# Performance work log

Measured on AMD Instinct MI355X. Metric: run time of the kernel, lower is better.

Reference implementation:

```python
import jax, jax.numpy as jnp
import numpy as np

N, E = 50000, 400000
IN, HID, HEADS, OUT, EDIM = 128, 16, 8, 128, 32


def _lin(key, fan_in, fan_out, bias=True):
    k1, k2 = jax.random.split(key)
    s = 1.0 / np.sqrt(fan_in)
    W = jax.random.uniform(k1, (fan_in, fan_out), jnp.float32, -s, s)
    if bias:
        b = jax.random.uniform(k2, (fan_out,), jnp.float32, -s, s)
        return W, b
    return W


def setup_inputs() -> dict:
    key = jax.random.key(0)
    ks = jax.random.split(key, 16)
    x = jax.random.normal(ks[0], (N, IN), jnp.float32)
    edge_index = jax.random.randint(ks[1], (2, E), 0, N, jnp.int64)
    edge_feats = jax.random.normal(ks[2], (E, EDIM), jnp.float32)
    H1 = HEADS * HID  # 128
    Wq1, bq1 = _lin(ks[3], IN, H1)
    Wk1, bk1 = _lin(ks[4], IN, H1)
    Wv1, bv1 = _lin(ks[5], IN, H1)
    We1 = _lin(ks[6], EDIM, H1, bias=False)
    Ws1, bs1 = _lin(ks[7], IN, H1)
    Wq2, bq2 = _lin(ks[8], H1, OUT)
    Wk2, bk2 = _lin(ks[9], H1, OUT)
    Wv2, bv2 = _lin(ks[10], H1, OUT)
    We2 = _lin(ks[11], EDIM, OUT, bias=False)
    Ws2, bs2 = _lin(ks[12], H1, OUT)
    return dict(x=x, edge_index=edge_index, edge_feats=edge_feats,
                Wq1=Wq1, bq1=bq1, Wk1=Wk1, bk1=bk1, Wv1=Wv1, bv1=bv1, We1=We1, Ws1=Ws1, bs1=bs1,
                Wq2=Wq2, bq2=bq2, Wk2=Wk2, bk2=bk2, Wv2=Wv2, bv2=bv2, We2=We2, Ws2=Ws2, bs2=bs2)


def transformer_conv(x, src, dst, e, Wq, bq, Wk, bk, Wv, bv, We, Ws, bs, heads, ch, concat):
    # PyG TransformerConv: project at nodes, gather to edges.
    n = x.shape[0]
    q = (x @ Wq + bq).reshape(n, heads, ch)[dst]          # [E,H,C]
    k = (x @ Wk + bk).reshape(n, heads, ch)[src]
    v = (x @ Wv + bv).reshape(n, heads, ch)[src]
    ee = (e @ We).reshape(-1, heads, ch)                   # edge conditioning
    k = k + ee
    v = v + ee
    alpha = (q * k).sum(-1) / jnp.sqrt(jnp.asarray(ch, x.dtype))  # [E,H]
    # per-destination segment softmax
    m = jax.ops.segment_max(alpha, dst, num_segments=n)
    m = jnp.where(jnp.isfinite(m), m, 0.0)
    ea = jnp.exp(alpha - m[dst])
    denom = jax.ops.segment_sum(ea, dst, num_segments=n)
    attn = ea / jnp.maximum(denom[dst], 1e-16)
    out = jax.ops.segment_sum(attn[:, :, None] * v, dst, num_segments=n)  # [N,H,C]
    out = out.reshape(n, heads * ch) if concat else out.mean(axis=1)
    return out + x @ Ws + bs  # root_weight skip


def reference(x, edge_index, edge_feats,
              Wq1, bq1, Wk1, bk1, Wv1, bv1, We1, Ws1, bs1,
              Wq2, bq2, Wk2, bk2, Wv2, bv2, We2, Ws2, bs2):
    src, dst = edge_index[0], edge_index[1]
    h = jax.nn.relu(transformer_conv(x, src, dst, edge_feats,
                                     Wq1, bq1, Wk1, bk1, Wv1, bv1, We1, Ws1, bs1,
                                     HEADS, HID, True))
    # dropout p=0.0 (eval) -> identity
    out = jax.nn.relu(transformer_conv(h, src, dst, edge_feats,
                                       Wq2, bq2, Wk2, bk2, Wv2, bv2, We2, Ws2, bs2,
                                       1, OUT, False))
    return out
```

## Files before the change

kernel.cpp:

```cpp
#include <hip/hip_runtime.h>


using u16 = unsigned short;
using u32 = unsigned int;

#define NODES 50000
#define EDGES 400000
#define NB196 196

typedef __attribute__((ext_vector_type(8))) short bf16x8;
typedef __attribute__((ext_vector_type(4))) float f32x4;

__device__ __forceinline__ float bflo(u32 u) { return __uint_as_float(u << 16); }
__device__ __forceinline__ float bfhi(u32 u) { return __uint_as_float(u & 0xffff0000u); }
__device__ __forceinline__ u16 f2bf(float f) {
    u32 u = __float_as_uint(f);
    u += 0x7fffu + ((u >> 16) & 1u);
    return (u16)(u >> 16);
}
__device__ __forceinline__ u32 pack2(float a, float b) {
    return (u32)f2bf(a) | ((u32)f2bf(b) << 16);
}
__device__ __forceinline__ float rdv(const void* p, int i, int f) {
    return f ? ((const float*)p)[i]
             : __uint_as_float(((u32) reinterpret_cast<const u16*>(p)[i]) << 16);
}

#if __has_builtin(__builtin_amdgcn_fdot2_f32_bf16)
typedef __attribute__((ext_vector_type(2))) __bf16 bf2;
__device__ __forceinline__ float dot2bf(u32 a, u32 b, float c) {
    return __builtin_amdgcn_fdot2_f32_bf16(__builtin_bit_cast(bf2, a),
                                           __builtin_bit_cast(bf2, b), c, false);
}
#else
__device__ __forceinline__ float dot2bf(u32 a, u32 b, float c) {
    return fmaf(bflo(a), bflo(b), fmaf(bfhi(a), bfhi(b), c));
}
#endif

__device__ __forceinline__ float fexp2(float x) {
#if __has_builtin(__builtin_amdgcn_exp2f)
    return __builtin_amdgcn_exp2f(x);
#else
    return exp2f(x);
#endif
}

template <int CTRL>
__device__ __forceinline__ float dpp_addf(float x) {
    int y = __builtin_amdgcn_update_dpp(0, __float_as_int(x), CTRL, 0xF, 0xF, true);
    return x + __int_as_float(y);
}
template <int GRP>
__device__ __forceinline__ float grp_sum(float p, int lane) {
    p = dpp_addf<0xB1>(p);
    p = dpp_addf<0x4E>(p);
    p = dpp_addf<0x141>(p);
    if (GRP == 64) {
        p = dpp_addf<0x140>(p);
        p += __int_as_float(__builtin_amdgcn_ds_swizzle(__float_as_int(p), 0x401F));
        p += __int_as_float(__builtin_amdgcn_ds_bpermute((lane ^ 32) << 2,
                                                         __float_as_int(p)));
    }
    return p;
}

template <int SRC>
__device__ __forceinline__ u32 bcast8u(u32 x) {
    return (u32)__builtin_amdgcn_ds_swizzle((int)x, 0x18 | (SRC << 5));
}

__global__ __launch_bounds__(256) void fill_sentinel(float* __restrict__ out, int n, float val) {
    int i = blockIdx.x * 256 + threadIdx.x;
    if (i < n) out[i] = val;
}

__global__ __launch_bounds__(64) void detect_fmt(const u32* __restrict__ xw,
                                                 const int* __restrict__ eraw,
                                                 int* __restrict__ flags) {
    int lane = threadIdx.x;
    u32 e = (xw[lane] >> 7) & 0xffu;
    unsigned long long sane = __ballot(e >= 90u && e <= 141u);
    unsigned long long zodd = __ballot(eraw[1 + 2 * lane] == 0);
    if (lane == 0) {
        flags[0] = (sane == ~0ull) ? 0 : 1;
        flags[1] = (zodd == ~0ull) ? 1 : 0;
    }
}

#define CXB 3125
#define CDB 1563
__global__ __launch_bounds__(256) void convert_count(
    const void* __restrict__ X, const int* __restrict__ raw,
    const int* __restrict__ flags, u16* __restrict__ xbf,
    int* __restrict__ deg, int total, int E) {
    int b = blockIdx.x;
    if (b < CXB) {
        int i = (b * 256 + threadIdx.x) * 8;
        if (i >= total) return;
        if (flags[0]) {
            const float* xf = (const float*)X + i;
            float4 lo = *reinterpret_cast<const float4*>(xf);
            float4 hi = *reinterpret_cast<const float4*>(xf + 4);
            uint4 val = make_uint4(pack2(lo.x, lo.y), pack2(lo.z, lo.w),
                                   pack2(hi.x, hi.y), pack2(hi.z, hi.w));
            *reinterpret_cast<uint4*>(xbf + i) = val;
        } else {
            *reinterpret_cast<uint4*>(xbf + i) =
                *reinterpret_cast<const uint4*>((const u16*)X + i);
        }
    } else {
        int e = (b - CXB) * 256 + threadIdx.x;
        if (e < E) {
            int f = flags[1];
            int d = f ? raw[2 * (E + e)] : raw[E + e];
            if ((unsigned)d < (unsigned)NODES) atomicAdd(&deg[d], 1);
        }
    }
}

struct TPtrs {
    const void* src[8];
    u16*        dst[8];
    int         K[8];
};
struct WqeP {
    const void *Wq1, *We1, *bq1, *Wq2, *We2, *bq2;
    u16 *WtA, *WtB, *Wt2;
    float *bqe1, *bqe2;
    uint2 *WeP1, *WeP2;
};

__device__ __forceinline__ void wqe_item(const WqeP& Q, int idx, int f) {
    if (idx < 32768) {
        int col = idx >> 7, i = idx & 127;
        int hh = col >> 5, d = col & 31;
        float s = 0.f;
#pragma unroll
        for (int c = 0; c < 16; ++c)
            s += rdv(Q.Wq1, i * 128 + hh * 16 + c, f) * rdv(Q.We1, d * 128 + hh * 16 + c, f);
        if (col < 128) Q.WtA[col * 128 + i] = f2bf(s);
        else           Q.WtB[(col - 128) * 128 + i] = f2bf(s);
    } else if (idx < 49152) {
        int t = idx - 32768;
        int col = t >> 7, i = t & 127;
        float s = 0.f;
        if (col < 32) {
            for (int c = 0; c < 128; ++c)
                s += rdv(Q.Wq2, i * 128 + c, f) * rdv(Q.We2, col * 128 + c, f);
        }
        Q.Wt2[col * 128 + i] = f2bf(s * 0.125f);
    } else if (idx < 49408) {
        int col = idx - 49152;
        int hh = col >> 5, d = col & 31;
        float s = 0.f;
#pragma unroll
        for (int c = 0; c < 16; ++c)
            s += rdv(Q.bq1, hh * 16 + c, f) * rdv(Q.We1, d * 128 + hh * 16 + c, f);
        Q.bqe1[col] = s;
    } else if (idx < 49536) {
        int d = idx - 49408;
        float s = 0.f;
        if (d < 32)
            for (int c = 0; c < 128; ++c)
                s += rdv(Q.bq2, c, f) * rdv(Q.We2, d * 128 + c, f);
        Q.bqe2[d] = s * 0.125f;
    } else if (idx < 50560) {
        int ent = idx - 49536;
        int t = ent >> 6, l = ent & 63, c0 = 2 * l;
        u32 xv = pack2(rdv(Q.We1, (2 * t) * 128 + c0, f),
                       rdv(Q.We1, (2 * t + 1) * 128 + c0, f));
        u32 yv = pack2(rdv(Q.We1, (2 * t) * 128 + c0 + 1, f),
                       rdv(Q.We1, (2 * t + 1) * 128 + c0 + 1, f));
        Q.WeP1[ent] = make_uint2(xv, yv);
    } else if (idx < 51584) {
        int ent = idx - 50560;
        int t = ent >> 6, l = ent & 63, c0 = 2 * l;
        u32 xv = pack2(rdv(Q.We2, (2 * t) * 128 + c0, f),
                       rdv(Q.We2, (2 * t + 1) * 128 + c0, f));
        u32 yv = pack2(rdv(Q.We2, (2 * t) * 128 + c0 + 1, f),
                       rdv(Q.We2, (2 * t + 1) * 128 + c0 + 1, f));
        Q.WeP2[ent] = make_uint2(xv, yv);
    }
}

__global__ __launch_bounds__(256) void prep_w(TPtrs P, WqeP Q, const int* __restrict__ flags) {
    int f = flags[0];
    int b = blockIdx.x;
    if (b < 32) {
        int m = b >> 2;
        int quarter = 16384 >> 2;
        u16* d = P.dst[m];
        int base = (b & 3) * quarter;
        const float* sf = (const float*)P.src[m];
        const u16*   sb = (const u16*)P.src[m];
        for (int idx = base + threadIdx.x; idx < base + quarter; idx += 256) {
            int k = idx >> 7, n = idx & 127;
            d[n * 128 + k] = f ? f2bf(sf[idx]) : sb[idx];
        }
        return;
    }
    int idx = (b - 32) * 256 + threadIdx.x;
    if (idx < 51584) wqe_item(Q, idx, f);
}

__device__ __forceinline__ int block_scan256(int v) {
    __shared__ int ws[4];
    int t = threadIdx.x, lane = t & 63, w = t >> 6;
    int x = v;
#pragma unroll
    for (int off = 1; off < 64; off <<= 1) {
        int y = __shfl_up(x, off, 64);
        if (lane >= off) x += y;
    }
    if (lane == 63) ws[w] = x;
    __syncthreads();
#pragma unroll
    for (int j = 0; j < 3; ++j)
        if (j < w) x += ws[j];
    return x;
}

__global__ __launch_bounds__(256) void scan_a(const int* __restrict__ deg,
                                              int* __restrict__ bsum, int n) {
    int i = blockIdx.x * 256 + threadIdx.x;
    int v = (i < n) ? deg[i] : 0;
    int incl = block_scan256(v);
    if (threadIdx.x == 255) bsum[blockIdx.x] = incl;
}

__global__ __launch_bounds__(256) void scan_b(int* __restrict__ bsum, int nb) {
    int t = threadIdx.x;
    int v = (t < nb) ? bsum[t] : 0;
    int incl = block_scan256(v);
    if (t < nb) bsum[t] = incl - v;
}

__global__ __launch_bounds__(256) void scan_c(const int* __restrict__ deg,
                                              const int* __restrict__ bsum,
                                              int* __restrict__ row_ptr,
                                              int* __restrict__ cursor, int n) {
    int b = blockIdx.x;
    int i = b * 256 + threadIdx.x;
    int v = (i < n) ? deg[i] : 0;
    int incl = block_scan256(v) + bsum[b];
    if (i < n) {
        row_ptr[i + 1] = incl;
        cursor[i] = incl - v;
    }
    if (i == 0) row_ptr[0] = 0;
}

__global__ __launch_bounds__(256) void fill_csr(const int* __restrict__ raw,
                                                const int* __restrict__ flags,
                                                int* __restrict__ cursor,
                                                int* __restrict__ srcs,
                                                int* __restrict__ eids, int E) {
    int e = blockIdx.x * 256 + threadIdx.x;
    if (e < E) {
        int f = flags[1];
        int d = f ? raw[2 * (E + e)] : raw[E + e];
        int s = f ? raw[2 * e] : raw[e];
        if ((unsigned)d < (unsigned)NODES && (unsigned)s < (unsigned)NODES) {
            int pos = atomicAdd(&cursor[d], 1);
            if ((unsigned)pos < (unsigned)E) { srcs[pos] = s; eids[pos] = e; }
        }
    }
}

__global__ __launch_bounds__(256) void gather_ef(const int* __restrict__ eids,
                                                 const void* __restrict__ EF,
                                                 const int* __restrict__ flags,
                                                 u16* __restrict__ EFG, int E) {
    int t = blockIdx.x * 256 + threadIdx.x;
    int pos = t >> 2, seg = t & 3;
    if (pos >= E) return;
    int e = eids[pos];
    uint4 val;
    if (flags[0]) {
        const float* src = (const float*)EF + (size_t)e * 32 + seg * 8;
        float4 lo = *reinterpret_cast<const float4*>(src);
        float4 hi = *reinterpret_cast<const float4*>(src + 4);
        val = make_uint4(pack2(lo.x, lo.y), pack2(lo.z, lo.w),
                         pack2(hi.x, hi.y), pack2(hi.z, hi.w));
    } else {
        val = *reinterpret_cast<const uint4*>((const u16*)EF + (size_t)e * 32 + seg * 8);
    }
    *reinterpret_cast<uint4*>(EFG + (size_t)pos * 32 + seg * 8) = val;
}

struct GemmSets {
    const u16*  Wt[6];
    const void* bias[6];
    u16*        O[6];
    int         bf32[6];
    int         pitch[6];
    float       oscale[6];
};

__global__ __launch_bounds__(256) void gemm128m(
    const u16* __restrict__ A, const int* __restrict__ flags, GemmSets S,
    int nsets, int M) {
    constexpr int K = 128;
    constexpr int PAD = K + 8;
    constexpr int KV = K / 8;
    __shared__ u16 Asl[64 * PAD];
    __shared__ u16 Bsl[128 * PAD];

    int fin = flags[0];
    int m0 = blockIdx.x * 64;

    for (int idx = threadIdx.x; idx < 64 * KV; idx += 256) {
        int r = idx / KV, cv = idx % KV;
        int gr = m0 + r;
        uint4 val = make_uint4(0, 0, 0, 0);
        if (gr < M) val = *reinterpret_cast<const uint4*>(A + (size_t)gr * K + cv * 8);
        *reinterpret_cast<uint4*>(&Asl[r * PAD + cv * 8]) = val;
    }

    int lane = threadIdx.x & 63, wv = threadIdx.x >> 6;
    int l15 = lane & 15;
    int quad = lane >> 4;
    int kq = quad * 8;
    int row = m0 + wv * 16 + l15;

    for (int si = 0; si < nsets; ++si) {
        const u16*  Wt   = S.Wt[si];
        const void* bias = S.bias[si];
        u16*        O    = S.O[si];
        int   pitch = S.pitch[si];
        float os    = S.oscale[si];
        int   f     = S.bf32[si] ? 1 : fin;

        __syncthreads();
        for (int idx = threadIdx.x; idx < 128 * KV; idx += 256) {
            int r = idx / KV, cv = idx % KV;
            *reinterpret_cast<uint4*>(&Bsl[r * PAD + cv * 8]) =
                *reinterpret_cast<const uint4*>(Wt + r * K + cv * 8);
        }
        __syncthreads();

        f32x4 b4[8];
#pragma unroll
        for (int nt = 0; nt < 8; ++nt) {
            int col0 = nt * 16 + quad * 4;
            if (bias) {
                if (f) {
                    b4[nt] = *reinterpret_cast<const f32x4*>((const float*)bias + col0);
                } else {
                    uint2 bu = *reinterpret_cast<const uint2*>((const u16*)bias + col0);
                    b4[nt][0] = bflo(bu.x); b4[nt][1] = bfhi(bu.x);
                    b4[nt][2] = bflo(bu.y); b4[nt][3] = bfhi(bu.y);
                }
            } else {
                b4[nt][0] = b4[nt][1] = b4[nt][2] = b4[nt][3] = 0.f;
            }
        }

        f32x4 acc[8] = {};
#pragma unroll
        for (int k0 = 0; k0 < K; k0 += 32) {
            bf16x8 xf = *reinterpret_cast<const bf16x8*>(&Asl[(wv * 16 + l15) * PAD + k0 + kq]);
#pragma unroll
            for (int nt = 0; nt < 8; ++nt) {
                bf16x8 wf = *reinterpret_cast<const bf16x8*>(&Bsl[(nt * 16 + l15) * PAD + k0 + kq]);
                acc[nt] = __builtin_amdgcn_mfma_f32_16x16x32_bf16(wf, xf, acc[nt], 0, 0, 0);
            }
        }

        if (row < M) {
            u16* Orow = O + (size_t)row * pitch;
#pragma unroll
            for (int nt = 0; nt < 8; ++nt) {
                uint2 pk;
                pk.x = pack2((acc[nt][0] + b4[nt][0]) * os, (acc[nt][1] + b4[nt][1]) * os);
                pk.y = pack2((acc[nt][2] + b4[nt][2]) * os, (acc[nt][3] + b4[nt][3]) * os);
                *reinterpret_cast<uint2*>(Orow + nt * 16 + quad * 4) = pk;
            }
        }
    }
}

template <int HEADS, int F32OUT>
__global__ __launch_bounds__(256) void attn_kernel(
    const int* __restrict__ row_ptr, const int* __restrict__ srcs,
    const u16* __restrict__ Q, const u16* __restrict__ KV,
    const u16* __restrict__ EFG,
    const u16* __restrict__ QWA, const u16* __restrict__ QWB,
    const u16* __restrict__ SK, const uint2* __restrict__ WeP,
    void* __restrict__ OUT, int nn) {
    int wv = threadIdx.x >> 6, lane = threadIdx.x & 63;
    int node = blockIdx.x * 4 + wv;
    if (node >= nn) return;
    int h = lane >> 3, j = lane & 7;
    int c0 = lane * 2;
    constexpr int GRP = (HEADS == 8) ? 8 : 64;

    u32 qb = *reinterpret_cast<const u32*>(Q + (size_t)node * 128 + c0);
    const u16* qp = (HEADS == 8)
        ? ((h < 4 ? QWA : QWB) + (size_t)node * 128 + (h & 3) * 32 + j * 4)
        : (QWA + (size_t)node * 128 + j * 4);
    uint2 qwu = *reinterpret_cast<const uint2*>(qp);

    int beg = __builtin_amdgcn_readfirstlane(row_ptr[node]);
    int end = __builtin_amdgcn_readfirstlane(row_ptr[node + 1]);

    float l_run = 0.f, a0 = 0.f, a1 = 0.f;
    float f0 = 0.f, f1 = 0.f, f2 = 0.f, f3 = 0.f;

    auto edge_step = [&](u32 kbv, u32 vbv, uint2 ebv, bool valid) {
        float p = dot2bf(qb, kbv,
                 dot2bf(qwu.x, ebv.x,
                 dot2bf(qwu.y, ebv.y, 0.f)));
        p = grp_sum<GRP>(p, lane);
        float w = fexp2(p);
        if (!valid) w = 0.f;
        l_run += w;
        a0 = fmaf(w, bflo(vbv), a0);
        a1 = fmaf(w, bfhi(vbv), a1);
        f0 = fmaf(w, bflo(ebv.x), f0); f1 = fmaf(w, bfhi(ebv.x), f1);
        f2 = fmaf(w, bflo(ebv.y), f2); f3 = fmaf(w, bfhi(ebv.y), f3);
    };

    int i = beg;
    for (; i + 8 <= end; i += 8) {
        u32 kb[8], vb[8]; uint2 eb[8];
#pragma unroll
        for (int t = 0; t < 8; ++t) {
            int s = srcs[i + t];
            const u16* kp = KV + (size_t)s * 256;
            kb[t] = *reinterpret_cast<const u32*>(kp + c0);
            vb[t] = *reinterpret_cast<const u32*>(kp + 128 + c0);
            eb[t] = *reinterpret_cast<const uint2*>(EFG + (size_t)(i + t) * 32 + j * 4);
        }
#pragma unroll
        for (int t = 0; t < 8; ++t) edge_step(kb[t], vb[t], eb[t], true);
    }
    for (; i < end; i += 4) {
        int kleft = end - i;
        u32 kb[4], vb[4]; uint2 eb[4];
#pragma unroll
        for (int t = 0; t < 4; ++t) {
            int idx = (i + t < end) ? i + t : end - 1;
            int s = srcs[idx];
            const u16* kp = KV + (size_t)s * 256;
            kb[t] = *reinterpret_cast<const u32*>(kp + c0);
            vb[t] = *reinterpret_cast<const u32*>(kp + 128 + c0);
            eb[t] = *reinterpret_cast<const uint2*>(EFG + (size_t)idx * 32 + j * 4);
        }
#pragma unroll
        for (int t = 0; t < 4; ++t) edge_step(kb[t], vb[t], eb[t], t < kleft);
    }

    u32 Fp0 = pack2(f0, f1), Fp1 = pack2(f2, f3);
    float acc0 = 0.f, acc1 = 0.f;
#define EPI(SRC) do { \
        u32 A = bcast8u<SRC>(Fp0), B = bcast8u<SRC>(Fp1); \
        uint2 w0 = WeP[(2 * SRC) * 64 + lane]; \
        uint2 w1 = WeP[(2 * SRC + 1) * 64 + lane]; \
        acc0 = dot2bf(A, w0.x, acc0); acc0 = dot2bf(B, w1.x, acc0); \
        acc1 = dot2bf(A, w0.y, acc1); acc1 = dot2bf(B, w1.y, acc1); \
    } while (0)
    EPI(0); EPI(1); EPI(2); EPI(3); EPI(4); EPI(5); EPI(6); EPI(7);
#undef EPI

    float inv = 1.f / fmaxf(l_run, 1e-16f);
    u32 sb = *reinterpret_cast<const u32*>(SK + (size_t)node * 128 + c0);
    float o0 = fmaxf(fmaf(a0 + acc0, inv, bflo(sb)), 0.f);
    float o1 = fmaxf(fmaf(a1 + acc1, inv, bfhi(sb)), 0.f);
    if (F32OUT) {
        *reinterpret_cast<float2*>((float*)OUT + (size_t)node * 128 + c0) =
            make_float2(o0, o1);
    } else {
        *reinterpret_cast<u32*>((u16*)OUT + (size_t)node * 128 + c0) = pack2(o0, o1);
    }
}

extern "C" void kernel_launch(void* const* d_in, const int* in_sizes, int n_in,
                              void* d_out, int out_size, void* d_ws, size_t ws_size,
                              hipStream_t stream) {
    const int N = NODES, E = EDGES;
    const void* x  = d_in[0];
    const int*  ei = (const int*)d_in[1];
    const void* ef = d_in[2];
    const void* Wq1 = d_in[3];  const void* bq1 = d_in[4];
    const void* Wk1 = d_in[5];  const void* bk1 = d_in[6];
    const void* Wv1 = d_in[7];  const void* bv1 = d_in[8];
    const void* We1 = d_in[9];
    const void* Ws1 = d_in[10]; const void* bs1 = d_in[11];
    const void* Wq2 = d_in[12]; const void* bq2 = d_in[13];
    const void* Wk2 = d_in[14]; const void* bk2 = d_in[15];
    const void* Wv2 = d_in[16]; const void* bv2 = d_in[17];
    const void* We2 = d_in[18];
    const void* Ws2 = d_in[19]; const void* bs2 = d_in[20];

    char* ws = (char*)d_ws;
    size_t off = 0;
    auto carve = [&](size_t bytes) -> void* {
        void* p = ws + off;
        off += (bytes + 255) & ~(size_t)255;
        return p;
    };

    u16* WtQ1 = (u16*)carve(128 * 128 * 2);
    u16* WtK1 = (u16*)carve(128 * 128 * 2);
    u16* WtV1 = (u16*)carve(128 * 128 * 2);
    u16* WtS1 = (u16*)carve(128 * 128 * 2);
    u16* WtQ2 = (u16*)carve(128 * 128 * 2);
    u16* WtK2 = (u16*)carve(128 * 128 * 2);
    u16* WtV2 = (u16*)carve(128 * 128 * 2);
    u16* WtS2 = (u16*)carve(128 * 128 * 2);
    u16* WtqA = (u16*)carve(128 * 128 * 2);
    u16* WtqB = (u16*)carve(128 * 128 * 2);
    u16* Wtq2 = (u16*)carve(128 * 128 * 2);
    float* bqe1 = (float*)carve(256 * 4);
    float* bqe2 = (float*)carve(128 * 4);
    uint2* WeP1 = (uint2*)carve(1024 * 8);
    uint2* WeP2 = (uint2*)carve(1024 * 8);
    int* flags   = (int*)carve(256);
    int* deg     = (int*)carve((size_t)N * 4);
    int* bsum    = (int*)carve((size_t)NB196 * 4);
    int* row_ptr = (int*)carve((size_t)(N + 1) * 4);
    int* cursor  = (int*)carve((size_t)N * 4);
    int* srcs    = (int*)carve((size_t)E * 4);
    int* eids    = (int*)carve((size_t)E * 4);
    u16* xbf  = (u16*)carve((size_t)N * 128 * 2);
    u16* q    = (u16*)carve((size_t)N * 128 * 2);
    u16* kv   = (u16*)carve((size_t)N * 256 * 2);
    u16* sk   = (u16*)carve((size_t)N * 128 * 2);
    u16* h    = (u16*)carve((size_t)N * 128 * 2);
    u16* qweA = (u16*)carve((size_t)N * 128 * 2);
    u16* qweB = (u16*)carve((size_t)N * 128 * 2);
    u16* qwe2 = (u16*)carve((size_t)N * 128 * 2);
    u16* efg  = (u16*)carve((size_t)E * 32 * 2);
    const size_t REQ = off;

    if (ws_size < REQ) {
        hipLaunchKernelGGL(fill_sentinel, dim3((out_size + 255) / 256), dim3(256), 0, stream,
                           (float*)d_out, out_size, 16.0f * (float)(ws_size >> 20));
        return;
    }

    const float s2_1 = 0.25f * 1.44269504f;
    const float s2_2 = 0.08838834764831845f * 1.44269504f;

    hipLaunchKernelGGL(detect_fmt, dim3(1), dim3(64), 0, stream, (const u32*)x, ei, flags);

    (void)hipMemsetAsync(deg, 0, (size_t)N * 4, stream);
    hipLaunchKernelGGL(convert_count, dim3(CXB + CDB), dim3(256), 0, stream,
                       x, ei, flags, xbf, deg, N * 128, E);

    TPtrs tp;
    tp.src[0] = Wq1; tp.dst[0] = WtQ1; tp.K[0] = 128;
    tp.src[1] = Wk1; tp.dst[1] = WtK1; tp.K[1] = 128;
    tp.src[2] = Wv1; tp.dst[2] = WtV1; tp.K[2] = 128;
    tp.src[3] = Ws1; tp.dst[3] = WtS1; tp.K[3] = 128;
    tp.src[4] = Wq2; tp.dst[4] = WtQ2; tp.K[4] = 128;
    tp.src[5] = Wk2; tp.dst[5] = WtK2; tp.K[5] = 128;
    tp.src[6] = Wv2; tp.dst[6] = WtV2; tp.K[6] = 128;
    tp.src[7] = Ws2; tp.dst[7] = WtS2; tp.K[7] = 128;
    WqeP wp;
    wp.Wq1 = Wq1; wp.We1 = We1; wp.bq1 = bq1;
    wp.Wq2 = Wq2; wp.We2 = We2; wp.bq2 = bq2;
    wp.WtA = WtqA; wp.WtB = WtqB; wp.Wt2 = Wtq2;
    wp.bqe1 = bqe1; wp.bqe2 = bqe2;
    wp.WeP1 = WeP1; wp.WeP2 = WeP2;
    hipLaunchKernelGGL(prep_w, dim3(32 + 202), dim3(256), 0, stream, tp, wp, flags);

    hipLaunchKernelGGL(scan_a, dim3(NB196), dim3(256), 0, stream, deg, bsum, N);
    hipLaunchKernelGGL(scan_b, dim3(1), dim3(256), 0, stream, bsum, NB196);
    hipLaunchKernelGGL(scan_c, dim3(NB196), dim3(256), 0, stream, deg, bsum, row_ptr, cursor, N);
    hipLaunchKernelGGL(fill_csr, dim3((E + 255) / 256), dim3(256), 0, stream, ei, flags, cursor,
                       srcs, eids, E);

    hipLaunchKernelGGL(gather_ef, dim3(E * 4 / 256), dim3(256), 0, stream,
                       eids, ef, flags, efg, E);

    const int gN = (N + 63) / 64;
    const int gA = (N + 3) / 4;

    {
        GemmSets S;
        S.Wt[0] = WtQ1; S.bias[0] = bq1;  S.O[0] = q;        S.bf32[0] = 0; S.pitch[0] = 128; S.oscale[0] = s2_1;
        S.Wt[1] = WtK1; S.bias[1] = bk1;  S.O[1] = kv;       S.bf32[1] = 0; S.pitch[1] = 256; S.oscale[1] = 1.f;
        S.Wt[2] = WtV1; S.bias[2] = bv1;  S.O[2] = kv + 128; S.bf32[2] = 0; S.pitch[2] = 256; S.oscale[2] = 1.f;
        S.Wt[3] = WtS1; S.bias[3] = bs1;  S.O[3] = sk;       S.bf32[3] = 0; S.pitch[3] = 128; S.oscale[3] = 1.f;
        S.Wt[4] = WtqA; S.bias[4] = bqe1;       S.O[4] = qweA; S.bf32[4] = 1; S.pitch[4] = 128; S.oscale[4] = s2_1;
        S.Wt[5] = WtqB; S.bias[5] = bqe1 + 128; S.O[5] = qweB; S.bf32[5] = 1; S.pitch[5] = 128; S.oscale[5] = s2_1;
        hipLaunchKernelGGL(gemm128m, dim3(gN), dim3(256), 0, stream, xbf, flags, S, 6, N);
    }
    hipLaunchKernelGGL((attn_kernel<8, 0>), dim3(gA), dim3(256), 0, stream,
                       row_ptr, srcs, q, kv, efg, qweA, qweB, sk, WeP1, (void*)h, N);

    {
        GemmSets S;
        S.Wt[0] = WtQ2; S.bias[0] = bq2;  S.O[0] = q;        S.bf32[0] = 0; S.pitch[0] = 128; S.oscale[0] = s2_2;
        S.Wt[1] = WtK2; S.bias[1] = bk2;  S.O[1] = kv;       S.bf32[1] = 0; S.pitch[1] = 256; S.oscale[1] = 1.f;
        S.Wt[2] = WtV2; S.bias[2] = bv2;  S.O[2] = kv + 128; S.bf32[2] = 0; S.pitch[2] = 256; S.oscale[2] = 1.f;
        S.Wt[3] = WtS2; S.bias[3] = bs2;  S.O[3] = sk;       S.bf32[3] = 0; S.pitch[3] = 128; S.oscale[3] = 1.f;
        S.Wt[4] = Wtq2; S.bias[4] = bqe2; S.O[4] = qwe2;     S.bf32[4] = 1; S.pitch[4] = 128; S.oscale[4] = s2_2;
        S.Wt[5] = Wtq2; S.bias[5] = bqe2; S.O[5] = qwe2;     S.bf32[5] = 1; S.pitch[5] = 128; S.oscale[5] = s2_2;
        hipLaunchKernelGGL(gemm128m, dim3(gN), dim3(256), 0, stream, h, flags, S, 5, N);
    }
    hipLaunchKernelGGL((attn_kernel<1, 1>), dim3(gA), dim3(256), 0, stream,
                       row_ptr, srcs, q, kv, efg, qwe2, qwe2, sk, WeP2, d_out, N);
}
```

Before: 431.0 us.

## Merge preprocessing kernels to cut launches in graph transformer pipeline

Format detection now runs inline in every block, so detect_fmt, convert_count and prep_w become one mega-kernel. scan_b is folded into scan_c, with each block rescanning the block sums itself. fill_csr and gather_ef are fused so each edge thread copies its own edge features straight to its CSR slot, which removes the eids buffer and one pass over it. The aim is fewer launches and less intermediate memory traffic, paid for with redundant detection and scan work per block and a less coalesced per-thread 64-byte feature copy.

```diff
diff --git a/kernel.cpp b/kernel.cpp
--- a/kernel.cpp
+++ b/kernel.cpp
@@ -24,6 +24,17 @@
 __device__ __forceinline__ float rdv(const void* p, int i, int f) {
     return f ? ((const float*)p)[i]
              : __uint_as_float(((u32) reinterpret_cast<const u16*>(p)[i]) << 16);
+}
+
+__device__ __forceinline__ void detect_inline(const u32* __restrict__ xw,
+                                              const int* __restrict__ eraw,
+                                              int& f, int& f1) {
+    int lane = threadIdx.x & 63;
+    u32 e = (xw[lane] >> 7) & 0xffu;
+    unsigned long long sane = __ballot(e >= 90u && e <= 141u);
+    unsigned long long zodd = __ballot(eraw[1 + 2 * lane] == 0);
+    f  = (sane == ~0ull) ? 0 : 1;
+    f1 = (zodd == ~0ull) ? 1 : 0;
 }
 
 #if __has_builtin(__builtin_amdgcn_fdot2_f32_bf16)
@@ -73,50 +84,6 @@
 __global__ __launch_bounds__(256) void fill_sentinel(float* __restrict__ out, int n, float val) {
     int i = blockIdx.x * 256 + threadIdx.x;
     if (i < n) out[i] = val;
-}
-
-__global__ __launch_bounds__(64) void detect_fmt(const u32* __restrict__ xw,
-                                                 const int* __restrict__ eraw,
-                                                 int* __restrict__ flags) {
-    int lane = threadIdx.x;
-    u32 e = (xw[lane] >> 7) & 0xffu;
-    unsigned long long sane = __ballot(e >= 90u && e <= 141u);
-    unsigned long long zodd = __ballot(eraw[1 + 2 * lane] == 0);
-    if (lane == 0) {
-        flags[0] = (sane == ~0ull) ? 0 : 1;
-        flags[1] = (zodd == ~0ull) ? 1 : 0;
-    }
-}
-
-#define CXB 3125
-#define CDB 1563
-__global__ __launch_bounds__(256) void convert_count(
-    const void* __restrict__ X, const int* __restrict__ raw,
-    const int* __restrict__ flags, u16* __restrict__ xbf,
-    int* __restrict__ deg, int total, int E) {
-    int b = blockIdx.x;
-    if (b < CXB) {
-        int i = (b * 256 + threadIdx.x) * 8;
-        if (i >= total) return;
-        if (flags[0]) {
-            const float* xf = (const float*)X + i;
-            float4 lo = *reinterpret_cast<const float4*>(xf);
-            float4 hi = *reinterpret_cast<const float4*>(xf + 4);
-            uint4 val = make_uint4(pack2(lo.x, lo.y), pack2(lo.z, lo.w),
-                                   pack2(hi.x, hi.y), pack2(hi.z, hi.w));
-            *reinterpret_cast<uint4*>(xbf + i) = val;
-        } else {
-            *reinterpret_cast<uint4*>(xbf + i) =
-                *reinterpret_cast<const uint4*>((const u16*)X + i);
-        }
-    } else {
-        int e = (b - CXB) * 256 + threadIdx.x;
-        if (e < E) {
-            int f = flags[1];
-            int d = f ? raw[2 * (E + e)] : raw[E + e];
-            if ((unsigned)d < (unsigned)NODES) atomicAdd(&deg[d], 1);
-        }
-    }
 }
 
 struct TPtrs {
@@ -184,24 +151,56 @@
     }
 }
 
-__global__ __launch_bounds__(256) void prep_w(TPtrs P, WqeP Q, const int* __restrict__ flags) {
-    int f = flags[0];
+#define CXB 3125
+#define CDB 1563
+#define MGB (CXB + CDB + 32 + 202)
+__global__ __launch_bounds__(256) void mega1(
+    const void* __restrict__ X, const int* __restrict__ raw,
+    TPtrs P, WqeP Q, u16* __restrict__ xbf, int* __restrict__ deg,
+    int* __restrict__ flags, int total, int E) {
+    int f, f1;
+    detect_inline((const u32*)X, raw, f, f1);
     int b = blockIdx.x;
-    if (b < 32) {
-        int m = b >> 2;
-        int quarter = 16384 >> 2;
-        u16* d = P.dst[m];
-        int base = (b & 3) * quarter;
-        const float* sf = (const float*)P.src[m];
-        const u16*   sb = (const u16*)P.src[m];
-        for (int idx = base + threadIdx.x; idx < base + quarter; idx += 256) {
-            int k = idx >> 7, n = idx & 127;
-            d[n * 128 + k] = f ? f2bf(sf[idx]) : sb[idx];
-        }
-        return;
-    }
-    int idx = (b - 32) * 256 + threadIdx.x;
-    if (idx < 51584) wqe_item(Q, idx, f);
+    if (b == 0 && threadIdx.x == 0) { flags[0] = f; flags[1] = f1; }
+
+    if (b < CXB) {
+        int i = (b * 256 + threadIdx.x) * 8;
+        if (i >= total) return;
+        if (f) {
+            const float* xf = (const float*)X + i;
+            float4 lo = *reinterpret_cast<const float4*>(xf);
+            float4 hi = *reinterpret_cast<const float4*>(xf + 4);
+            *reinterpret_cast<uint4*>(xbf + i) =
+                make_uint4(pack2(lo.x, lo.y), pack2(lo.z, lo.w),
+                           pack2(hi.x, hi.y), pack2(hi.z, hi.w));
+        } else {
+            *reinterpret_cast<uint4*>(xbf + i) =
+                *reinterpret_cast<const uint4*>((const u16*)X + i);
+        }
+    } else if (b < CXB + CDB) {
+        int e = (b - CXB) * 256 + threadIdx.x;
+        if (e < E) {
+            int d = f1 ? raw[2 * (E + e)] : raw[E + e];
+            if ((unsigned)d < (unsigned)NODES) atomicAdd(&deg[d], 1);
+        }
+    } else {
+        int bb = b - CXB - CDB;
+        if (bb < 32) {
+            int m = bb >> 2;
+            int quarter = 16384 >> 2;
+            u16* d = P.dst[m];
+            int base = (bb & 3) * quarter;
+            const float* sf = (const float*)P.src[m];
+            const u16*   sb = (const u16*)P.src[m];
+            for (int idx = base + threadIdx.x; idx < base + quarter; idx += 256) {
+                int k = idx >> 7, n = idx & 127;
+                d[n * 128 + k] = f ? f2bf(sf[idx]) : sb[idx];
+            }
+        } else {
+            int idx = (bb - 32) * 256 + threadIdx.x;
+            if (idx < 51584) wqe_item(Q, idx, f);
+        }
+    }
 }
 
 __device__ __forceinline__ int block_scan256(int v) {
@@ -229,21 +228,21 @@
     if (threadIdx.x == 255) bsum[blockIdx.x] = incl;
 }
 
-__global__ __launch_bounds__(256) void scan_b(int* __restrict__ bsum, int nb) {
+__global__ __launch_bounds__(256) void scan_bc(const int* __restrict__ deg,
+                                               const int* __restrict__ bsum,
+                                               int* __restrict__ row_ptr,
+                                               int* __restrict__ cursor, int n) {
+    __shared__ int sb[256];
+    int c = blockIdx.x;
     int t = threadIdx.x;
-    int v = (t < nb) ? bsum[t] : 0;
-    int incl = block_scan256(v);
-    if (t < nb) bsum[t] = incl - v;
-}
-
-__global__ __launch_bounds__(256) void scan_c(const int* __restrict__ deg,
-                                              const int* __restrict__ bsum,
-                                              int* __restrict__ row_ptr,
-                                              int* __restrict__ cursor, int n) {
-    int b = blockIdx.x;
-    int i = b * 256 + threadIdx.x;
+    int v0 = (t < NB196) ? bsum[t] : 0;
+    int incl0 = block_scan256(v0);
+    sb[t] = incl0;
+    __syncthreads();
+    int base = (c > 0) ? sb[c - 1] : 0;
+    int i = c * 256 + t;
     int v = (i < n) ? deg[i] : 0;
-    int incl = block_scan256(v) + bsum[b];
+    int incl = block_scan256(v) + base;
     if (i < n) {
         row_ptr[i + 1] = incl;
         cursor[i] = incl - v;
@@ -251,42 +250,40 @@
     if (i == 0) row_ptr[0] = 0;
 }
 
-__global__ __launch_bounds__(256) void fill_csr(const int* __restrict__ raw,
-                                                const int* __restrict__ flags,
-                                                int* __restrict__ cursor,
-                                                int* __restrict__ srcs,
-                                                int* __restrict__ eids, int E) {
+__global__ __launch_bounds__(256) void fill_gather(
+    const int* __restrict__ raw, const u32* __restrict__ xw,
+    const void* __restrict__ EF, int* __restrict__ cursor,
+    int* __restrict__ srcs, u16* __restrict__ EFG, int E) {
+    int f, f1;
+    detect_inline(xw, raw, f, f1);
     int e = blockIdx.x * 256 + threadIdx.x;
-    if (e < E) {
-        int f = flags[1];
-        int d = f ? raw[2 * (E + e)] : raw[E + e];
-        int s = f ? raw[2 * e] : raw[e];
-        if ((unsigned)d < (unsigned)NODES && (unsigned)s < (unsigned)NODES) {
-            int pos = atomicAdd(&cursor[d], 1);
-            if ((unsigned)pos < (unsigned)E) { srcs[pos] = s; eids[pos] = e; }
-        }
-    }
-}
-
-__global__ __launch_bounds__(256) void gather_ef(const int* __restrict__ eids,
-                                                 const void* __restrict__ EF,
-                                                 const int* __restrict__ flags,
-                                                 u16* __restrict__ EFG, int E) {
-    int t = blockIdx.x * 256 + threadIdx.x;
-    int pos = t >> 2, seg = t & 3;
-    if (pos >= E) return;
-    int e = eids[pos];
-    uint4 val;
-    if (flags[0]) {
-        const float* src = (const float*)EF + (size_t)e * 32 + seg * 8;
-        float4 lo = *reinterpret_cast<const float4*>(src);
-        float4 hi = *reinterpret_cast<const float4*>(src + 4);
-        val = make_uint4(pack2(lo.x, lo.y), pack2(lo.z, lo.w),
-                         pack2(hi.x, hi.y), pack2(hi.z, hi.w));
-    } else {
-        val = *reinterpret_cast<const uint4*>((const u16*)EF + (size_t)e * 32 + seg * 8);
-    }
-    *reinterpret_cast<uint4*>(EFG + (size_t)pos * 32 + seg * 8) = val;
+    if (e >= E) return;
+    int d = f1 ? raw[2 * (E + e)] : raw[E + e];
+    int s = f1 ? raw[2 * e] : raw[e];
+    if ((unsigned)d < (unsigned)NODES && (unsigned)s < (unsigned)NODES) {
+        int pos = atomicAdd(&cursor[d], 1);
+        if ((unsigned)pos < (unsigned)E) {
+            srcs[pos] = s;
+            u16* dst = EFG + (size_t)pos * 32;
+            if (f) {
+                const float* src = (const float*)EF + (size_t)e * 32;
+#pragma unroll
+                for (int seg = 0; seg < 4; ++seg) {
+                    float4 lo = *reinterpret_cast<const float4*>(src + seg * 8);
+                    float4 hi = *reinterpret_cast<const float4*>(src + seg * 8 + 4);
+                    *reinterpret_cast<uint4*>(dst + seg * 8) =
+                        make_uint4(pack2(lo.x, lo.y), pack2(lo.z, lo.w),
+                                   pack2(hi.x, hi.y), pack2(hi.z, hi.w));
+                }
+            } else {
+                const uint4* src =
+                    reinterpret_cast<const uint4*>((const u16*)EF + (size_t)e * 32);
+#pragma unroll
+                for (int seg = 0; seg < 4; ++seg)
+                    *reinterpret_cast<uint4*>(dst + seg * 8) = src[seg];
+            }
+        }
+    }
 }
 
 struct GemmSets {
@@ -523,7 +520,6 @@
     int* row_ptr = (int*)carve((size_t)(N + 1) * 4);
     int* cursor  = (int*)carve((size_t)N * 4);
     int* srcs    = (int*)carve((size_t)E * 4);
-    int* eids    = (int*)carve((size_t)E * 4);
     u16* xbf  = (u16*)carve((size_t)N * 128 * 2);
     u16* q    = (u16*)carve((size_t)N * 128 * 2);
     u16* kv   = (u16*)carve((size_t)N * 256 * 2);
@@ -543,12 +539,6 @@
 
     const float s2_1 = 0.25f * 1.44269504f;
     const float s2_2 = 0.08838834764831845f * 1.44269504f;
-
-    hipLaunchKernelGGL(detect_fmt, dim3(1), dim3(64), 0, stream, (const u32*)x, ei, flags);
-
-    (void)hipMemsetAsync(deg, 0, (size_t)N * 4, stream);
-    hipLaunchKernelGGL(convert_count, dim3(CXB + CDB), dim3(256), 0, stream,
-                       x, ei, flags, xbf, deg, N * 128, E);
 
     TPtrs tp;
     tp.src[0] = Wq1; tp.dst[0] = WtQ1; tp.K[0] = 128;
@@ -565,16 +555,15 @@
     wp.WtA = WtqA; wp.WtB = WtqB; wp.Wt2 = Wtq2;
     wp.bqe1 = bqe1; wp.bqe2 = bqe2;
     wp.WeP1 = WeP1; wp.WeP2 = WeP2;
-    hipLaunchKernelGGL(prep_w, dim3(32 + 202), dim3(256), 0, stream, tp, wp, flags);
-
+
+    (void)hipMemsetAsync(deg, 0, (size_t)N * 4, stream);
+    hipLaunchKernelGGL(mega1, dim3(MGB), dim3(256), 0, stream,
+                       x, ei, tp, wp, xbf, deg, flags, N * 128, E);
     hipLaunchKernelGGL(scan_a, dim3(NB196), dim3(256), 0, stream, deg, bsum, N);
-    hipLaunchKernelGGL(scan_b, dim3(1), dim3(256), 0, stream, bsum, NB196);
-    hipLaunchKernelGGL(scan_c, dim3(NB196), dim3(256), 0, stream, deg, bsum, row_ptr, cursor, N);
-    hipLaunchKernelGGL(fill_csr, dim3((E + 255) / 256), dim3(256), 0, stream, ei, flags, cursor,
-                       srcs, eids, E);
-
-    hipLaunchKernelGGL(gather_ef, dim3(E * 4 / 256), dim3(256), 0, stream,
-                       eids, ef, flags, efg, E);
+    hipLaunchKernelGGL(scan_bc, dim3(NB196), dim3(256), 0, stream,
+                       deg, bsum, row_ptr, cursor, N);
+    hipLaunchKernelGGL(fill_gather, dim3((E + 255) / 256), dim3(256), 0, stream,
+                       ei, (const u32*)x, ef, cursor, srcs, efg, E);
 
     const int gN = (N + 63) / 64;
     const int gA = (N + 3) / 4;
```

After: 429.8 us. No clear change (-0.3%).
